# Kernel optimization log

Hardware: AMD Instinct MI355X
Metric: run time of the kernel (lower is better)

The kernel has to match this reference:

```python
import jax, jax.numpy as jnp
import numpy as np

TEMP = 0.1
K = 4
EPS = 1e-12


def _normalize(x):
    return x / jnp.maximum(jnp.linalg.norm(x, axis=1, keepdims=True), 1e-12)


def _sq_dists(a, b):
    # a: [Na,3], b: [Nb,3] -> [Na,Nb] squared euclidean distances
    aa = jnp.sum(a * a, axis=1, keepdims=True)          # [Na,1]
    bb = jnp.sum(b * b, axis=1, keepdims=True).T        # [1,Nb]
    return aa + bb - 2.0 * (a @ b.T)


def _directional_loss(f_q, f_db, d2_q_db):
    # knn of each query point in the database cloud, then cosine-sim softmax self-consistency loss
    _, idx = jax.lax.top_k(-d2_q_db, K)                  # [Nq,K] nearest-db indices
    f_matched = f_db[idx]                                # [Nq,K,C] gather (pointops.grouping)
    sim = jnp.einsum('nc,nkc->nk', f_q, f_matched) / TEMP
    p = jax.nn.softmax(sim, axis=1)                      # q_i == softmax when use_sinkhorn=False
    return jnp.mean(-jnp.log(jnp.sum(p * p, axis=1) + EPS))


def setup_inputs() -> dict:
    key = jax.random.key(0)
    k1, k2, k3, k4 = jax.random.split(key, 4)
    return {
        'feat_i': jax.random.normal(k1, (20000, 96), dtype=jnp.float32),
        'coord_i': jax.random.uniform(k2, (20000, 3), dtype=jnp.float32),
        'feat_j': jax.random.normal(k3, (10000, 96), dtype=jnp.float32),
        'coord_j': jax.random.uniform(k4, (10000, 3), dtype=jnp.float32),
    }


def reference(feat_i, coord_i, feat_j, coord_j):
    fi = _normalize(feat_i)
    fj = _normalize(feat_j)
    d2 = _sq_dists(coord_i, coord_j)                     # [Ni,Nj]
    loss_i = _directional_loss(fi, fj, d2)               # i queries, j database
    loss_j = _directional_loss(fj, fi, d2.T)             # j queries, i database
    pair = (loss_i + loss_j) * 0.5
    # num_views = 2 -> total_loss / max(1, num_views - 1) = pair
    return pair
```

## Files before the change

### kernel.cpp

```cpp
#include <hip/hip_runtime.h>
#include <math.h>

#define KMASK 0xFFFF8000u
#define IMASK 0x7FFFu

__device__ __forceinline__ float wave_reduce_sum(float v) {
    #pragma unroll
    for (int off = 32; off >= 1; off >>= 1) v += __shfl_xor(v, off, 64);
    return v;
}

__device__ __forceinline__ unsigned wave_min_u32(unsigned v) {
    #pragma unroll
    for (int off = 32; off >= 1; off >>= 1) {
        unsigned o = (unsigned)__shfl_xor((int)v, off, 64);
        v = (o < v) ? o : v;
    }
    return v;
}

__device__ __forceinline__ unsigned gmin8(unsigned v) {
    #pragma unroll
    for (int off = 4; off >= 1; off >>= 1) {
        unsigned o = (unsigned)__shfl_xor((int)v, off, 64);
        v = (o < v) ? o : v;
    }
    return v;
}
__device__ __forceinline__ float gsum8(float v) {
    #pragma unroll
    for (int off = 4; off >= 1; off >>= 1) v += __shfl_xor(v, off, 64);
    return v;
}

__device__ __forceinline__ void insert4kv(unsigned k, unsigned v,
                                          unsigned (&bk)[4], unsigned (&bv)[4]) {
    const bool c0 = k < bk[0], c1 = k < bk[1], c2 = k < bk[2], c3 = k < bk[3];
    bk[3] = c2 ? bk[2] : (c3 ? k : bk[3]);
    bv[3] = c2 ? bv[2] : (c3 ? v : bv[3]);
    bk[2] = c1 ? bk[1] : (c2 ? k : bk[2]);
    bv[2] = c1 ? bv[1] : (c2 ? v : bv[2]);
    bk[1] = c0 ? bk[0] : (c1 ? k : bk[1]);
    bv[1] = c0 ? bv[0] : (c1 ? v : bv[1]);
    bk[0] = c0 ? k : bk[0];
    bv[0] = c0 ? v : bv[0];
}

__device__ __forceinline__ int cell_of(float x, int G) {
    int c = (int)(x * (float)G);
    return (c < 0) ? 0 : ((c >= G) ? G - 1 : c);
}

__device__ __forceinline__ float dot4(float4 a, float4 b) {
    return fmaf(a.w, b.w, fmaf(a.z, b.z, fmaf(a.y, b.y, a.x * b.x)));
}


__global__ __launch_bounds__(256)
void grid_zero(int* __restrict__ stA, int nA, int* __restrict__ stB, int nB,
               float* __restrict__ out)
{
    const int t = blockIdx.x * 256 + threadIdx.x;
    if (t < nA) stA[t] = 0;
    if (t < nB) stB[t] = 0;
    if (t == 0) out[0] = 0.0f;
}

__global__ __launch_bounds__(256)
void grid_count(const float* __restrict__ cA, int nA, int GA, int* __restrict__ stA,
                const float* __restrict__ cB, int nB, int GB, int* __restrict__ stB)
{
    const int t = blockIdx.x * 256 + threadIdx.x;
    const float* c; int* s; int G; int p;
    if (t < nA)           { c = cA; s = stA; G = GA; p = t; }
    else if (t < nA + nB) { c = cB; s = stB; G = GB; p = t - nA; }
    else return;
    const int cx = cell_of(c[3*p], G), cy = cell_of(c[3*p+1], G), cz = cell_of(c[3*p+2], G);
    atomicAdd(&s[(cz * G + cy) * G + cx + 1], 1);
}

__global__ __launch_bounds__(256)
void grid_scan(int* __restrict__ sA, int nA, int* __restrict__ cuA,
               int* __restrict__ sB, int nB, int* __restrict__ cuB)
{
    int* s  = blockIdx.x ? sB  : sA;
    int* cu = blockIdx.x ? cuB : cuA;
    const int n = blockIdx.x ? nB : nA;
    __shared__ int part[256];
    const int t = threadIdx.x;
    const int len = n + 1;
    const int chunk = (len + 255) >> 8;
    const int lo = t * chunk;
    const int hi = (lo + chunk < len) ? (lo + chunk) : len;
    int sum = 0;
    for (int i = lo; i < hi; ++i) sum += s[i];
    part[t] = sum;
    __syncthreads();
    for (int d = 1; d < 256; d <<= 1) {
        const int v = (t >= d) ? part[t - d] : 0;
        __syncthreads();
        part[t] += v;
        __syncthreads();
    }
    int run = (t > 0) ? part[t - 1] : 0;
    for (int i = lo; i < hi; ++i) {
        run += s[i];
        s[i] = run;
        if (i < n) cu[i] = run;
    }
}

__global__ __launch_bounds__(256)
void grid_scatter(const float* __restrict__ cA, int nA, int GA, int* __restrict__ cuA,
                  float4* __restrict__ soA,
                  const float* __restrict__ cB, int nB, int GB, int* __restrict__ cuB,
                  float4* __restrict__ soB)
{
    const int t = blockIdx.x * 256 + threadIdx.x;
    const float* c; int* cu; float4* so; int G; int p;
    if (t < nA)           { c = cA; cu = cuA; so = soA; G = GA; p = t; }
    else if (t < nA + nB) { c = cB; cu = cuB; so = soB; G = GB; p = t - nA; }
    else return;
    const float x = c[3*p], y = c[3*p+1], z = c[3*p+2];
    const int cx = cell_of(x, G), cy = cell_of(y, G), cz = cell_of(z, G);
    const int pos = atomicAdd(&cu[(cz * G + cy) * G + cx], 1);
    so[pos] = make_float4(x, y, z, __uint_as_float((unsigned)p));
}


__global__ __launch_bounds__(256)
void knnloss(const float* __restrict__ fi, int Ni,
             const float* __restrict__ fj, int Nj,
             const float4* __restrict__ soA, const int* __restrict__ stA, int GA,
             const float4* __restrict__ soB, const int* __restrict__ stB, int GB,
             float sc0, float sc1, float* __restrict__ out)
{
    const int sub = threadIdx.x & 7;
    const int qid = (blockIdx.x * 256 + threadIdx.x) >> 3;
    float acc = 0.0f;

    if (qid < Ni + Nj) {
        const bool d0 = (qid < Ni);
        const int sq = d0 ? qid : qid - Ni;
        const float4* soq = d0 ? soB : soA;
        const float4* so = d0 ? soA : soB;
        const int*    st = d0 ? stA : stB;
        const int      G = d0 ? GA  : GB;
        const int     nd = d0 ? Nj  : Ni;
        const float*  fd = d0 ? fj  : fi;
        const float scale = d0 ? sc0 : sc1;

        const float4 Q = soq[sq];
        const unsigned p = __float_as_uint(Q.w);
        const float* fqp = (d0 ? fi : fj) + (size_t)p * 96;

        const float4* q4 = (const float4*)fqp;
        const float4 qa = q4[3*sub], qb = q4[3*sub+1], qc = q4[3*sub+2];

        const float qx = Q.x, qy = Q.y, qz = Q.z;
        const float h = 1.0f / (float)G;
        const int cx = cell_of(qx, G), cy = cell_of(qy, G), cz = cell_of(qz, G);
        unsigned nk[4], nv[4];

        {
            const int x0 = max(cx - 1, 0), x1 = min(cx + 1, G - 1);
            int csr[9], cer[9];
            #pragma unroll
            for (int dz = 0; dz < 3; ++dz) {
                #pragma unroll
                for (int dy = 0; dy < 3; ++dy) {
                    const int zz = cz + dz - 1, yy = cy + dy - 1;
                    const bool v = ((unsigned)zz < (unsigned)G) & ((unsigned)yy < (unsigned)G);
                    const int rb = v ? (zz * G + yy) * G : 0;
                    csr[dz*3+dy] = v ? st[rb + x0] : 0;
                    cer[dz*3+dy] = v ? st[rb + x1 + 1] : 0;
                }
            }
            unsigned bk[4] = {~0u, ~0u, ~0u, ~0u};
            unsigned bv[4] = {~0u, ~0u, ~0u, ~0u};
            #pragma unroll
            for (int r = 0; r < 9; ++r) {
                const int ce = cer[r];
                for (int cc = csr[r] + sub; cc < ce; cc += 16) {
                    const float4 P0 = so[cc];
                    const int cc1 = cc + 8;
                    const bool v1 = (cc1 < ce);
                    float4 P1 = P0;
                    if (v1) P1 = so[cc1];
                    const float dx0 = P0.x - qx, dy0 = P0.y - qy, dz0 = P0.z - qz;
                    const float d20 = fmaf(dx0, dx0, fmaf(dy0, dy0, dz0 * dz0));
                    const unsigned k0 = (__float_as_uint(d20) & KMASK) | (unsigned)cc;
                    insert4kv(k0, __float_as_uint(P0.w), bk, bv);
                    const float dx1 = P1.x - qx, dy1 = P1.y - qy, dz1 = P1.z - qz;
                    const float d21 = fmaf(dx1, dx1, fmaf(dy1, dy1, dz1 * dz1));
                    unsigned k1 = (__float_as_uint(d21) & KMASK) | (unsigned)cc1;
                    if (!v1) k1 = ~0u;
                    insert4kv(k1, __float_as_uint(P1.w), bk, bv);
                }
            }
            unsigned k0 = bk[0], k1 = bk[1], k2 = bk[2], k3 = bk[3];
            unsigned v0 = bv[0], v1 = bv[1], v2 = bv[2], v3 = bv[3];
            #pragma unroll
            for (int r = 0; r < 4; ++r) {
                const unsigned m = gmin8(k0);
                const bool win = (k0 == m);
                nv[r] = gmin8(win ? v0 : ~0u);
                nk[r] = m;
                k0 = win ? k1 : k0; v0 = win ? v1 : v0;
                k1 = win ? k2 : k1; v1 = win ? v2 : v1;
                k2 = win ? k3 : k2; v2 = win ? v3 : v2;
                k3 = win ? ~0u : k3;
            }
            const int y0 = max(cy - 1, 0), y1 = min(cy + 1, G - 1);
            const int z0 = max(cz - 1, 0), z1 = min(cz + 1, G - 1);
            float margin = 3.0e38f;
            if (x0 > 0)     margin = fminf(margin, qx - (float)x0 * h);
            if (x1 < G - 1) margin = fminf(margin, (float)(x1 + 1) * h - qx);
            if (y0 > 0)     margin = fminf(margin, qy - (float)y0 * h);
            if (y1 < G - 1) margin = fminf(margin, (float)(y1 + 1) * h - qy);
            if (z0 > 0)     margin = fminf(margin, qz - (float)z0 * h);
            if (z1 < G - 1) margin = fminf(margin, (float)(z1 + 1) * h - qz);
            const bool covered = (margin > 1.0e37f);
            const float kd = __uint_as_float(nk[3] & KMASK);
            const bool ok = covered || (kd * 1.01f <= margin * margin);

            if (!ok) {
                for (int s = 2; ; ++s) {
                    const int sx0 = max(cx - s, 0), sx1 = min(cx + s, G - 1);
                    const int sy0 = max(cy - s, 0), sy1 = min(cy + s, G - 1);
                    const int sz0 = max(cz - s, 0), sz1 = min(cz + s, G - 1);
                    unsigned b2k[4] = {~0u, ~0u, ~0u, ~0u};
                    unsigned b2v[4] = {~0u, ~0u, ~0u, ~0u};
                    for (int z = sz0; z <= sz1; ++z) {
                        for (int y = sy0; y <= sy1; ++y) {
                            const int rb = (z * G + y) * G;
                            const int cs = st[rb + sx0];
                            const int ce = st[rb + sx1 + 1];
                            for (int cc = cs + sub; cc < ce; cc += 8) {
                                const float4 P = so[cc];
                                const float dx = P.x - qx, dy = P.y - qy, dz = P.z - qz;
                                const float d2 = fmaf(dx, dx, fmaf(dy, dy, dz * dz));
                                const unsigned k =
                                    (__float_as_uint(d2) & KMASK) | (unsigned)cc;
                                insert4kv(k, __float_as_uint(P.w), b2k, b2v);
                            }
                        }
                    }
                    unsigned u0 = b2k[0], u1 = b2k[1], u2 = b2k[2], u3 = b2k[3];
                    unsigned w0 = b2v[0], w1 = b2v[1], w2 = b2v[2], w3 = b2v[3];
                    #pragma unroll
                    for (int r = 0; r < 4; ++r) {
                        const unsigned m = gmin8(u0);
                        const bool win = (u0 == m);
                        nv[r] = gmin8(win ? w0 : ~0u);
                        nk[r] = m;
                        u0 = win ? u1 : u0; w0 = win ? w1 : w0;
                        u1 = win ? u2 : u1; w1 = win ? w2 : w1;
                        u2 = win ? u3 : u2; w2 = win ? w3 : w2;
                        u3 = win ? ~0u : u3;
                    }
                    float mg = 3.0e38f;
                    if (sx0 > 0)     mg = fminf(mg, qx - (float)sx0 * h);
                    if (sx1 < G - 1) mg = fminf(mg, (float)(sx1 + 1) * h - qx);
                    if (sy0 > 0)     mg = fminf(mg, qy - (float)sy0 * h);
                    if (sy1 < G - 1) mg = fminf(mg, (float)(sy1 + 1) * h - qy);
                    if (sz0 > 0)     mg = fminf(mg, qz - (float)sz0 * h);
                    if (sz1 < G - 1) mg = fminf(mg, (float)(sz1 + 1) * h - qz);
                    const bool cov = (mg > 1.0e37f);
                    const float k2d = __uint_as_float(nk[3] & KMASK);
                    if (cov || (k2d * 1.01f <= mg * mg)) break;
                }
            }
        }

        const unsigned nm1 = (unsigned)(nd - 1);
        const unsigned i0 = nv[0] < nm1 ? nv[0] : nm1;
        const unsigned i1 = nv[1] < nm1 ? nv[1] : nm1;
        const unsigned i2 = nv[2] < nm1 ? nv[2] : nm1;
        const unsigned i3 = nv[3] < nm1 ? nv[3] : nm1;

        const float4* f0 = (const float4*)(fd + (size_t)i0 * 96);
        const float4* f1 = (const float4*)(fd + (size_t)i1 * 96);
        const float4* f2 = (const float4*)(fd + (size_t)i2 * 96);
        const float4* f3 = (const float4*)(fd + (size_t)i3 * 96);
        const float4 a0 = f0[3*sub], b0 = f0[3*sub+1], c0 = f0[3*sub+2];
        const float4 a1 = f1[3*sub], b1 = f1[3*sub+1], c1 = f1[3*sub+2];
        const float4 a2 = f2[3*sub], b2 = f2[3*sub+1], c2 = f2[3*sub+2];
        const float4 a3 = f3[3*sub], b3 = f3[3*sub+1], c3 = f3[3*sub+2];

        const float ssq = gsum8(dot4(qa,qa) + dot4(qb,qb) + dot4(qc,qc));

        float sim[4];
        {
            const float dv = gsum8(dot4(qa,a0) + dot4(qb,b0) + dot4(qc,c0));
            const float sd = gsum8(dot4(a0,a0) + dot4(b0,b0) + dot4(c0,c0));
            sim[0] = dv * rsqrtf(fmaxf(ssq, 1e-24f) * fmaxf(sd, 1e-24f)) * 10.0f;
        }
        {
            const float dv = gsum8(dot4(qa,a1) + dot4(qb,b1) + dot4(qc,c1));
            const float sd = gsum8(dot4(a1,a1) + dot4(b1,b1) + dot4(c1,c1));
            sim[1] = dv * rsqrtf(fmaxf(ssq, 1e-24f) * fmaxf(sd, 1e-24f)) * 10.0f;
        }
        {
            const float dv = gsum8(dot4(qa,a2) + dot4(qb,b2) + dot4(qc,c2));
            const float sd = gsum8(dot4(a2,a2) + dot4(b2,b2) + dot4(c2,c2));
            sim[2] = dv * rsqrtf(fmaxf(ssq, 1e-24f) * fmaxf(sd, 1e-24f)) * 10.0f;
        }
        {
            const float dv = gsum8(dot4(qa,a3) + dot4(qb,b3) + dot4(qc,c3));
            const float sd = gsum8(dot4(a3,a3) + dot4(b3,b3) + dot4(c3,c3));
            sim[3] = dv * rsqrtf(fmaxf(ssq, 1e-24f) * fmaxf(sd, 1e-24f)) * 10.0f;
        }

        const float m = fmaxf(fmaxf(sim[0], sim[1]), fmaxf(sim[2], sim[3]));
        const float e0 = __expf(sim[0] - m), e1 = __expf(sim[1] - m);
        const float e2 = __expf(sim[2] - m), e3 = __expf(sim[3] - m);
        const float ssum = e0 + e1 + e2 + e3;
        const float inv = 1.0f / ssum;
        const float p2 = (e0*e0 + e1*e1 + e2*e2 + e3*e3) * inv * inv;
        if (sub == 0) acc = -__logf(p2 + 1e-12f) * scale;
    }

    acc = wave_reduce_sum(acc);
    __shared__ float red[4];
    if ((threadIdx.x & 63) == 0) red[threadIdx.x >> 6] = acc;
    __syncthreads();
    if (threadIdx.x == 0) atomicAdd(out, red[0] + red[1] + red[2] + red[3]);
}


#define WPB 4
__device__ __forceinline__ void insert4u(unsigned k, unsigned (&b)[4]) {
    const bool c0 = k < b[0], c1 = k < b[1], c2 = k < b[2], c3 = k < b[3];
    b[3] = c2 ? b[2] : (c3 ? k : b[3]);
    b[2] = c1 ? b[1] : (c2 ? k : b[2]);
    b[1] = c0 ? b[0] : (c1 ? k : b[1]);
    b[0] = c0 ? k : b[0];
}

template<int QPW>
__device__ __forceinline__ void brute_dir(
    const float* __restrict__ cq, const float* __restrict__ fq, int Nq,
    const float* __restrict__ cd, const float* __restrict__ fd, int Nd,
    float scale, float* __restrict__ out, int blk)
{
    const int lane = threadIdx.x & 63;
    const int widx = threadIdx.x >> 6;
    int qbase = (blk * WPB + widx) * QPW;
    if (qbase >= Nq) return;
    qbase = __builtin_amdgcn_readfirstlane(qbase);

    float qx[QPW], qy[QPW], qz[QPW];
    #pragma unroll
    for (int q = 0; q < QPW; ++q) {
        const int qi = (qbase + q < Nq) ? (qbase + q) : (Nq - 1);
        qx[q] = cq[qi*3]; qy[q] = cq[qi*3+1]; qz[q] = cq[qi*3+2];
    }
    unsigned bk[QPW][4];
    #pragma unroll
    for (int q = 0; q < QPW; ++q) {
        #pragma unroll
        for (int k = 0; k < 4; ++k) bk[q][k] = ~0u;
    }
    for (int base = 0; base < Nd; base += 64) {
        const int p = base + lane;
        const int cp = (p < Nd) ? p : (Nd - 1);
        const float px = cd[cp*3], py = cd[cp*3+1], pz = cd[cp*3+2];
        #pragma unroll
        for (int q = 0; q < QPW; ++q) {
            const float dx = px - qx[q], dy = py - qy[q], dz = pz - qz[q];
            const float d2 = dx*dx + dy*dy + dz*dz;
            unsigned k = (__float_as_uint(d2) & KMASK) | (unsigned)p;
            if (p >= Nd) k = ~0u;
            insert4u(k, bk[q]);
        }
    }
    float wacc = 0.0f;
    #pragma unroll
    for (int q = 0; q < QPW; ++q) {
        if (qbase + q >= Nq) break;
        unsigned t0 = bk[q][0], t1 = bk[q][1], t2 = bk[q][2], t3 = bk[q][3];
        int ni_[4];
        #pragma unroll
        for (int k = 0; k < 4; ++k) {
            const unsigned m = wave_min_u32(t0);
            ni_[k] = (int)(m & IMASK);
            const bool win = (t0 == m);
            t0 = win ? t1 : t0; t1 = win ? t2 : t1; t2 = win ? t3 : t2; t3 = win ? ~0u : t3;
        }
        const float* fqp = fq + (size_t)(qbase + q) * 96;
        const float qf0 = fqp[lane];
        const float qf1 = (lane < 32) ? fqp[64 + lane] : 0.0f;
        const float ssq = wave_reduce_sum(qf0*qf0 + qf1*qf1);
        float sim[4];
        #pragma unroll
        for (int k = 0; k < 4; ++k) {
            const float* fdp = fd + (size_t)ni_[k] * 96;
            const float df0 = fdp[lane];
            const float df1 = (lane < 32) ? fdp[64 + lane] : 0.0f;
            const float dotv = wave_reduce_sum(qf0*df0 + qf1*df1);
            const float ssd = wave_reduce_sum(df0*df0 + df1*df1);
            sim[k] = dotv * rsqrtf(fmaxf(ssq, 1e-24f) * fmaxf(ssd, 1e-24f)) * 10.0f;
        }
        const float m = fmaxf(fmaxf(sim[0], sim[1]), fmaxf(sim[2], sim[3]));
        const float e0 = __expf(sim[0]-m), e1 = __expf(sim[1]-m);
        const float e2 = __expf(sim[2]-m), e3 = __expf(sim[3]-m);
        const float ssum = e0+e1+e2+e3;
        const float inv = 1.0f/ssum;
        const float p2 = (e0*e0+e1*e1+e2*e2+e3*e3)*inv*inv;
        wacc += -__logf(p2 + 1e-12f);
    }
    if (lane == 0) atomicAdd(out, wacc * scale);
}

__global__ __launch_bounds__(256)
void brute_fused(const float* __restrict__ ci, const float* __restrict__ fi, int Ni,
                 const float* __restrict__ cj, const float* __restrict__ fj, int Nj,
                 float s0, float s1, int B0, int B1, float* __restrict__ out)
{
    const int bid = (int)blockIdx.x;
    const int bmin = (B0 < B1) ? B0 : B1;
    int dir, blk;
    if (bid < 2 * bmin) { dir = bid & 1; blk = bid >> 1; }
    else { dir = (B0 > B1) ? 0 : 1; blk = bid - bmin; }
    if (dir == 0) brute_dir<8>(ci, fi, Ni, cj, fj, Nj, s0, out, blk);
    else          brute_dir<4>(cj, fj, Nj, ci, fi, Ni, s1, out, blk);
}


extern "C" void kernel_launch(void* const* d_in, const int* in_sizes, int n_in,
                              void* d_out, int out_size, void* d_ws, size_t ws_size,
                              hipStream_t stream) {
    const float* feat_i  = (const float*)d_in[0];
    const float* coord_i = (const float*)d_in[1];
    const float* feat_j  = (const float*)d_in[2];
    const float* coord_j = (const float*)d_in[3];
    const int Ni = in_sizes[0] / 96;
    const int Nj = in_sizes[2] / 96;
    float* out = (float*)d_out;

    auto gridfor = [](int n) {
        int g = (int)cbrtf((float)n / 4.5f);
        if (g < 2) g = 2;
        if (g > 28) g = 28;
        return g;
    };
    const int GA = gridfor(Nj), GB = gridfor(Ni);
    const int GA3 = GA * GA * GA, GB3 = GB * GB * GB;

    size_t off = 0;
    auto alloc = [&](size_t bytes) { size_t o = off; off = (off + bytes + 15) & ~(size_t)15; return o; };
    const size_t o_soA  = alloc((size_t)Nj * 16);
    const size_t o_soB  = alloc((size_t)Ni * 16);
    const size_t o_stA  = alloc((size_t)(GA3 + 1) * 4);
    const size_t o_stB  = alloc((size_t)(GB3 + 1) * 4);
    const size_t o_cuA  = alloc((size_t)GA3 * 4);
    const size_t o_cuB  = alloc((size_t)GB3 * 4);

    if (ws_size >= off && Ni >= 16 && Nj >= 16 && Ni <= 32000 && Nj <= 32000) {
        char* W = (char*)d_ws;
        float4* soA = (float4*)(W + o_soA);
        float4* soB = (float4*)(W + o_soB);
        int* stA = (int*)(W + o_stA);
        int* stB = (int*)(W + o_stB);
        int* cuA = (int*)(W + o_cuA);
        int* cuB = (int*)(W + o_cuB);

        const int nPts = Ni + Nj;
        const int nmax = ((GA3 > GB3) ? GA3 : GB3) + 1;

        grid_zero<<<(nmax + 255) / 256, 256, 0, stream>>>(stA, GA3 + 1, stB, GB3 + 1, out);
        grid_count<<<(nPts + 255) / 256, 256, 0, stream>>>(
            coord_j, Nj, GA, stA, coord_i, Ni, GB, stB);
        grid_scan<<<2, 256, 0, stream>>>(stA, GA3, cuA, stB, GB3, cuB);
        grid_scatter<<<(nPts + 255) / 256, 256, 0, stream>>>(
            coord_j, Nj, GA, cuA, soA, coord_i, Ni, GB, cuB, soB);

        const int nQ = Ni + Nj;
        const int nblk = (nQ * 8 + 255) / 256;
        knnloss<<<nblk, 256, 0, stream>>>(
            feat_i, Ni, feat_j, Nj,
            soA, stA, GA, soB, stB, GB,
            0.5f / (float)Ni, 0.5f / (float)Nj, out);
    } else {
        hipMemsetAsync(out, 0, sizeof(float), stream);
        const int waves0 = (Ni + 7) / 8;
        const int B0 = (waves0 + WPB - 1) / WPB;
        const int waves1 = (Nj + 3) / 4;
        const int B1 = (waves1 + WPB - 1) / WPB;
        brute_fused<<<B0 + B1, 256, 0, stream>>>(
            coord_i, feat_i, Ni, coord_j, feat_j, Nj,
            0.5f / (float)Ni, 0.5f / (float)Nj, B0, B1, out);
    }
}
```

Baseline: 49.56 us.

## Reorder feature rows into grid-sorted order during scatter and drop value tracking

The scatter kernel now copies each point's 96-float feature row into a cell-sorted buffer alongside its coordinates. The kNN loss kernel then reads query and neighbor features by sorted index, so the top-4 selection only needs the packed distance|sorted-index keys and no longer carries a parallel payload array or the extra shuffle-min per neighbor. This should improve locality of the feature gathers and cut register and shuffle pressure. In exchange it adds a full extra read and write of both feature arrays (about 11.5 MB) in the scatter kernel.

```diff
diff --git a/kernel.cpp b/kernel.cpp
--- a/kernel.cpp
+++ b/kernel.cpp
@@ -33,17 +33,12 @@
     return v;
 }
 
-__device__ __forceinline__ void insert4kv(unsigned k, unsigned v,
-                                          unsigned (&bk)[4], unsigned (&bv)[4]) {
-    const bool c0 = k < bk[0], c1 = k < bk[1], c2 = k < bk[2], c3 = k < bk[3];
-    bk[3] = c2 ? bk[2] : (c3 ? k : bk[3]);
-    bv[3] = c2 ? bv[2] : (c3 ? v : bv[3]);
-    bk[2] = c1 ? bk[1] : (c2 ? k : bk[2]);
-    bv[2] = c1 ? bv[1] : (c2 ? v : bv[2]);
-    bk[1] = c0 ? bk[0] : (c1 ? k : bk[1]);
-    bv[1] = c0 ? bv[0] : (c1 ? v : bv[1]);
-    bk[0] = c0 ? k : bk[0];
-    bv[0] = c0 ? v : bv[0];
+__device__ __forceinline__ void insert4u(unsigned k, unsigned (&b)[4]) {
+    const bool c0 = k < b[0], c1 = k < b[1], c2 = k < b[2], c3 = k < b[3];
+    b[3] = c2 ? b[2] : (c3 ? k : b[3]);
+    b[2] = c1 ? b[1] : (c2 ? k : b[2]);
+    b[1] = c0 ? b[0] : (c1 ? k : b[1]);
+    b[0] = c0 ? k : b[0];
 }
 
 __device__ __forceinline__ int cell_of(float x, int G) {
@@ -111,28 +106,35 @@
 }
 
 __global__ __launch_bounds__(256)
-void grid_scatter(const float* __restrict__ cA, int nA, int GA, int* __restrict__ cuA,
-                  float4* __restrict__ soA,
-                  const float* __restrict__ cB, int nB, int GB, int* __restrict__ cuB,
-                  float4* __restrict__ soB)
+void grid_scatter(const float* __restrict__ cA, const float* __restrict__ fA,
+                  int nA, int GA, int* __restrict__ cuA,
+                  float4* __restrict__ soA, float4* __restrict__ fsA,
+                  const float* __restrict__ cB, const float* __restrict__ fB,
+                  int nB, int GB, int* __restrict__ cuB,
+                  float4* __restrict__ soB, float4* __restrict__ fsB)
 {
     const int t = blockIdx.x * 256 + threadIdx.x;
-    const float* c; int* cu; float4* so; int G; int p;
-    if (t < nA)           { c = cA; cu = cuA; so = soA; G = GA; p = t; }
-    else if (t < nA + nB) { c = cB; cu = cuB; so = soB; G = GB; p = t - nA; }
+    const float* c; const float* f; int* cu; float4* so; float4* fs; int G; int p;
+    if (t < nA)           { c = cA; f = fA; cu = cuA; so = soA; fs = fsA; G = GA; p = t; }
+    else if (t < nA + nB) { c = cB; f = fB; cu = cuB; so = soB; fs = fsB; G = GB; p = t - nA; }
     else return;
     const float x = c[3*p], y = c[3*p+1], z = c[3*p+2];
     const int cx = cell_of(x, G), cy = cell_of(y, G), cz = cell_of(z, G);
     const int pos = atomicAdd(&cu[(cz * G + cy) * G + cx], 1);
     so[pos] = make_float4(x, y, z, __uint_as_float((unsigned)p));
-}
-
-
-__global__ __launch_bounds__(256)
-void knnloss(const float* __restrict__ fi, int Ni,
-             const float* __restrict__ fj, int Nj,
-             const float4* __restrict__ soA, const int* __restrict__ stA, int GA,
-             const float4* __restrict__ soB, const int* __restrict__ stB, int GB,
+    const float4* src = (const float4*)(f + (size_t)p * 96);
+    float4* dst = fs + (size_t)pos * 24;
+    #pragma unroll
+    for (int k = 0; k < 24; ++k) dst[k] = src[k];
+}
+
+
+__global__ __launch_bounds__(256)
+void knnloss(const float4* __restrict__ fsA, const float4* __restrict__ soA,
+             const int* __restrict__ stA, int GA,
+             const float4* __restrict__ fsB, const float4* __restrict__ soB,
+             const int* __restrict__ stB, int GB,
+             int Ni, int Nj,
              float sc0, float sc1, float* __restrict__ out)
 {
     const int sub = threadIdx.x & 7;
@@ -143,24 +145,23 @@
         const bool d0 = (qid < Ni);
         const int sq = d0 ? qid : qid - Ni;
         const float4* soq = d0 ? soB : soA;
-        const float4* so = d0 ? soA : soB;
+        const float4* fqs = d0 ? fsB : fsA;
+        const float4* so  = d0 ? soA : soB;
+        const float4* fds = d0 ? fsA : fsB;
         const int*    st = d0 ? stA : stB;
         const int      G = d0 ? GA  : GB;
         const int     nd = d0 ? Nj  : Ni;
-        const float*  fd = d0 ? fj  : fi;
         const float scale = d0 ? sc0 : sc1;
 
         const float4 Q = soq[sq];
-        const unsigned p = __float_as_uint(Q.w);
-        const float* fqp = (d0 ? fi : fj) + (size_t)p * 96;
-
-        const float4* q4 = (const float4*)fqp;
+
+        const float4* q4 = fqs + (size_t)sq * 24;
         const float4 qa = q4[3*sub], qb = q4[3*sub+1], qc = q4[3*sub+2];
 
         const float qx = Q.x, qy = Q.y, qz = Q.z;
         const float h = 1.0f / (float)G;
         const int cx = cell_of(qx, G), cy = cell_of(qy, G), cz = cell_of(qz, G);
-        unsigned nk[4], nv[4];
+        unsigned nk[4];
 
         {
             const int x0 = max(cx - 1, 0), x1 = min(cx + 1, G - 1);
@@ -177,7 +178,6 @@
                 }
             }
             unsigned bk[4] = {~0u, ~0u, ~0u, ~0u};
-            unsigned bv[4] = {~0u, ~0u, ~0u, ~0u};
             #pragma unroll
             for (int r = 0; r < 9; ++r) {
                 const int ce = cer[r];
@@ -189,26 +189,23 @@
                     if (v1) P1 = so[cc1];
                     const float dx0 = P0.x - qx, dy0 = P0.y - qy, dz0 = P0.z - qz;
                     const float d20 = fmaf(dx0, dx0, fmaf(dy0, dy0, dz0 * dz0));
-                    const unsigned k0 = (__float_as_uint(d20) & KMASK) | (unsigned)cc;
-                    insert4kv(k0, __float_as_uint(P0.w), bk, bv);
+                    insert4u((__float_as_uint(d20) & KMASK) | (unsigned)cc, bk);
                     const float dx1 = P1.x - qx, dy1 = P1.y - qy, dz1 = P1.z - qz;
                     const float d21 = fmaf(dx1, dx1, fmaf(dy1, dy1, dz1 * dz1));
                     unsigned k1 = (__float_as_uint(d21) & KMASK) | (unsigned)cc1;
                     if (!v1) k1 = ~0u;
-                    insert4kv(k1, __float_as_uint(P1.w), bk, bv);
+                    insert4u(k1, bk);
                 }
             }
             unsigned k0 = bk[0], k1 = bk[1], k2 = bk[2], k3 = bk[3];
-            unsigned v0 = bv[0], v1 = bv[1], v2 = bv[2], v3 = bv[3];
             #pragma unroll
             for (int r = 0; r < 4; ++r) {
                 const unsigned m = gmin8(k0);
+                nk[r] = m;
                 const bool win = (k0 == m);
-                nv[r] = gmin8(win ? v0 : ~0u);
-                nk[r] = m;
-                k0 = win ? k1 : k0; v0 = win ? v1 : v0;
-                k1 = win ? k2 : k1; v1 = win ? v2 : v1;
-                k2 = win ? k3 : k2; v2 = win ? v3 : v2;
+                k0 = win ? k1 : k0;
+                k1 = win ? k2 : k1;
+                k2 = win ? k3 : k2;
                 k3 = win ? ~0u : k3;
             }
             const int y0 = max(cy - 1, 0), y1 = min(cy + 1, G - 1);
@@ -229,8 +226,7 @@
                     const int sx0 = max(cx - s, 0), sx1 = min(cx + s, G - 1);
                     const int sy0 = max(cy - s, 0), sy1 = min(cy + s, G - 1);
                     const int sz0 = max(cz - s, 0), sz1 = min(cz + s, G - 1);
-                    unsigned b2k[4] = {~0u, ~0u, ~0u, ~0u};
-                    unsigned b2v[4] = {~0u, ~0u, ~0u, ~0u};
+                    unsigned b2[4] = {~0u, ~0u, ~0u, ~0u};
                     for (int z = sz0; z <= sz1; ++z) {
                         for (int y = sy0; y <= sy1; ++y) {
                             const int rb = (z * G + y) * G;
@@ -240,23 +236,19 @@
                                 const float4 P = so[cc];
                                 const float dx = P.x - qx, dy = P.y - qy, dz = P.z - qz;
                                 const float d2 = fmaf(dx, dx, fmaf(dy, dy, dz * dz));
-                                const unsigned k =
-                                    (__float_as_uint(d2) & KMASK) | (unsigned)cc;
-                                insert4kv(k, __float_as_uint(P.w), b2k, b2v);
+                                insert4u((__float_as_uint(d2) & KMASK) | (unsigned)cc, b2);
                             }
                         }
                     }
-                    unsigned u0 = b2k[0], u1 = b2k[1], u2 = b2k[2], u3 = b2k[3];
-                    unsigned w0 = b2v[0], w1 = b2v[1], w2 = b2v[2], w3 = b2v[3];
+                    unsigned u0 = b2[0], u1 = b2[1], u2 = b2[2], u3 = b2[3];
                     #pragma unroll
                     for (int r = 0; r < 4; ++r) {
                         const unsigned m = gmin8(u0);
+                        nk[r] = m;
                         const bool win = (u0 == m);
-                        nv[r] = gmin8(win ? w0 : ~0u);
-                        nk[r] = m;
-                        u0 = win ? u1 : u0; w0 = win ? w1 : w0;
-                        u1 = win ? u2 : u1; w1 = win ? w2 : w1;
-                        u2 = win ? u3 : u2; w2 = win ? w3 : w2;
+                        u0 = win ? u1 : u0;
+                        u1 = win ? u2 : u1;
+                        u2 = win ? u3 : u2;
                         u3 = win ? ~0u : u3;
                     }
                     float mg = 3.0e38f;
@@ -274,41 +266,41 @@
         }
 
         const unsigned nm1 = (unsigned)(nd - 1);
-        const unsigned i0 = nv[0] < nm1 ? nv[0] : nm1;
-        const unsigned i1 = nv[1] < nm1 ? nv[1] : nm1;
-        const unsigned i2 = nv[2] < nm1 ? nv[2] : nm1;
-        const unsigned i3 = nv[3] < nm1 ? nv[3] : nm1;
-
-        const float4* f0 = (const float4*)(fd + (size_t)i0 * 96);
-        const float4* f1 = (const float4*)(fd + (size_t)i1 * 96);
-        const float4* f2 = (const float4*)(fd + (size_t)i2 * 96);
-        const float4* f3 = (const float4*)(fd + (size_t)i3 * 96);
-        const float4 a0 = f0[3*sub], b0 = f0[3*sub+1], c0 = f0[3*sub+2];
-        const float4 a1 = f1[3*sub], b1 = f1[3*sub+1], c1 = f1[3*sub+2];
-        const float4 a2 = f2[3*sub], b2 = f2[3*sub+1], c2 = f2[3*sub+2];
-        const float4 a3 = f3[3*sub], b3 = f3[3*sub+1], c3 = f3[3*sub+2];
+        unsigned i0 = nk[0] & IMASK; i0 = i0 < nm1 ? i0 : nm1;
+        unsigned i1 = nk[1] & IMASK; i1 = i1 < nm1 ? i1 : nm1;
+        unsigned i2 = nk[2] & IMASK; i2 = i2 < nm1 ? i2 : nm1;
+        unsigned i3 = nk[3] & IMASK; i3 = i3 < nm1 ? i3 : nm1;
+
+        const float4* f0 = fds + (size_t)i0 * 24;
+        const float4* f1 = fds + (size_t)i1 * 24;
+        const float4* f2 = fds + (size_t)i2 * 24;
+        const float4* f3 = fds + (size_t)i3 * 24;
+        const float4 a0 = f0[3*sub], b0 = f0[3*sub+1], c0f = f0[3*sub+2];
+        const float4 a1 = f1[3*sub], b1 = f1[3*sub+1], c1f = f1[3*sub+2];
+        const float4 a2 = f2[3*sub], b2 = f2[3*sub+1], c2f = f2[3*sub+2];
+        const float4 a3 = f3[3*sub], b3 = f3[3*sub+1], c3f = f3[3*sub+2];
 
         const float ssq = gsum8(dot4(qa,qa) + dot4(qb,qb) + dot4(qc,qc));
 
         float sim[4];
         {
-            const float dv = gsum8(dot4(qa,a0) + dot4(qb,b0) + dot4(qc,c0));
-            const float sd = gsum8(dot4(a0,a0) + dot4(b0,b0) + dot4(c0,c0));
+            const float dv = gsum8(dot4(qa,a0) + dot4(qb,b0) + dot4(qc,c0f));
+            const float sd = gsum8(dot4(a0,a0) + dot4(b0,b0) + dot4(c0f,c0f));
             sim[0] = dv * rsqrtf(fmaxf(ssq, 1e-24f) * fmaxf(sd, 1e-24f)) * 10.0f;
         }
         {
-            const float dv = gsum8(dot4(qa,a1) + dot4(qb,b1) + dot4(qc,c1));
-            const float sd = gsum8(dot4(a1,a1) + dot4(b1,b1) + dot4(c1,c1));
+            const float dv = gsum8(dot4(qa,a1) + dot4(qb,b1) + dot4(qc,c1f));
+            const float sd = gsum8(dot4(a1,a1) + dot4(b1,b1) + dot4(c1f,c1f));
             sim[1] = dv * rsqrtf(fmaxf(ssq, 1e-24f) * fmaxf(sd, 1e-24f)) * 10.0f;
         }
         {
-            const float dv = gsum8(dot4(qa,a2) + dot4(qb,b2) + dot4(qc,c2));
-            const float sd = gsum8(dot4(a2,a2) + dot4(b2,b2) + dot4(c2,c2));
+            const float dv = gsum8(dot4(qa,a2) + dot4(qb,b2) + dot4(qc,c2f));
+            const float sd = gsum8(dot4(a2,a2) + dot4(b2,b2) + dot4(c2f,c2f));
             sim[2] = dv * rsqrtf(fmaxf(ssq, 1e-24f) * fmaxf(sd, 1e-24f)) * 10.0f;
         }
         {
-            const float dv = gsum8(dot4(qa,a3) + dot4(qb,b3) + dot4(qc,c3));
-            const float sd = gsum8(dot4(a3,a3) + dot4(b3,b3) + dot4(c3,c3));
+            const float dv = gsum8(dot4(qa,a3) + dot4(qb,b3) + dot4(qc,c3f));
+            const float sd = gsum8(dot4(a3,a3) + dot4(b3,b3) + dot4(c3f,c3f));
             sim[3] = dv * rsqrtf(fmaxf(ssq, 1e-24f) * fmaxf(sd, 1e-24f)) * 10.0f;
         }
 
@@ -330,7 +322,7 @@
 
 
 #define WPB 4
-__device__ __forceinline__ void insert4u(unsigned k, unsigned (&b)[4]) {
+__device__ __forceinline__ void insert4u2(unsigned k, unsigned (&b)[4]) {
     const bool c0 = k < b[0], c1 = k < b[1], c2 = k < b[2], c3 = k < b[3];
     b[3] = c2 ? b[2] : (c3 ? k : b[3]);
     b[2] = c1 ? b[1] : (c2 ? k : b[2]);
@@ -372,7 +364,7 @@
             const float d2 = dx*dx + dy*dy + dz*dz;
             unsigned k = (__float_as_uint(d2) & KMASK) | (unsigned)p;
             if (p >= Nd) k = ~0u;
-            insert4u(k, bk[q]);
+            insert4u2(k, bk[q]);
         }
     }
     float wacc = 0.0f;
@@ -452,6 +444,8 @@
     auto alloc = [&](size_t bytes) { size_t o = off; off = (off + bytes + 15) & ~(size_t)15; return o; };
     const size_t o_soA  = alloc((size_t)Nj * 16);
     const size_t o_soB  = alloc((size_t)Ni * 16);
+    const size_t o_fsA  = alloc((size_t)Nj * 384);
+    const size_t o_fsB  = alloc((size_t)Ni * 384);
     const size_t o_stA  = alloc((size_t)(GA3 + 1) * 4);
     const size_t o_stB  = alloc((size_t)(GB3 + 1) * 4);
     const size_t o_cuA  = alloc((size_t)GA3 * 4);
@@ -461,6 +455,8 @@
         char* W = (char*)d_ws;
         float4* soA = (float4*)(W + o_soA);
         float4* soB = (float4*)(W + o_soB);
+        float4* fsA = (float4*)(W + o_fsA);
+        float4* fsB = (float4*)(W + o_fsB);
         int* stA = (int*)(W + o_stA);
         int* stB = (int*)(W + o_stB);
         int* cuA = (int*)(W + o_cuA);
@@ -474,14 +470,14 @@
             coord_j, Nj, GA, stA, coord_i, Ni, GB, stB);
         grid_scan<<<2, 256, 0, stream>>>(stA, GA3, cuA, stB, GB3, cuB);
         grid_scatter<<<(nPts + 255) / 256, 256, 0, stream>>>(
-            coord_j, Nj, GA, cuA, soA, coord_i, Ni, GB, cuB, soB);
+            coord_j, feat_j, Nj, GA, cuA, soA, fsA,
+            coord_i, feat_i, Ni, GB, cuB, soB, fsB);
 
         const int nQ = Ni + Nj;
         const int nblk = (nQ * 8 + 255) / 256;
         knnloss<<<nblk, 256, 0, stream>>>(
-            feat_i, Ni, feat_j, Nj,
-            soA, stA, GA, soB, stB, GB,
-            0.5f / (float)Ni, 0.5f / (float)Nj, out);
+            fsA, soA, stA, GA, fsB, soB, stB, GB,
+            Ni, Nj, 0.5f / (float)Ni, 0.5f / (float)Nj, out);
     } else {
         hipMemsetAsync(out, 0, sizeof(float), stream);
         const int waves0 = (Ni + 7) / 8;
```

Measured after the change: 64.95 us. 1.31x slower.
